# Optimization experiments

Hardware: AMD Instinct MI355X
Metric: run time of the kernel (lower is better)

## Reference

```python
import jax, jax.numpy as jnp
import numpy as np

B, C, H, W = 16, 8, 512, 512
EPS_TH = 1e-14

def setup_inputs() -> dict:
    key = jax.random.key(0)
    x = jax.random.normal(key, (B, C, H, W), dtype=jnp.float32)
    alpha = jnp.full((1,), 0.95, dtype=jnp.float32)
    beta = jnp.full((1,), 8.0, dtype=jnp.float32)
    return {"x": x, "alpha": alpha, "beta": beta}

def reference(x, alpha, beta):
    b, c, h, w = x.shape
    x2 = x.reshape(b * c, h * w)
    # torch.nanquantile with default linear interpolation == jnp.nanquantile
    i1 = jnp.nanquantile(x2, 0.01, axis=1, keepdims=True)   # [B*C, 1]
    i99 = jnp.nanquantile(x2, 0.99, axis=1, keepdims=True)  # [B*C, 1]
    th = (i1 + (i99 - i1) * alpha).reshape(b, c, 1, 1)      # broadcast instead of tile
    mask = (th > EPS_TH).astype(x.dtype)
    th_new = th * mask + (1.0 - mask)
    gate = 1.0 / (1.0 + jnp.exp(-(beta / th_new * (jnp.abs(x) - th * mask))))
    return jax.nn.relu(x) * gate
```

## Files before the change

kernel.cpp:

```cpp
#include <hip/hip_runtime.h>


#define ROWS 128
#define NPR  262144
#define BINS 8192
#define SHIFT 19
#define CAP  4096
#define HTPB 256
#define HBPR 8
#define QTPB 1024
#define OTPB 256

#define K_LO 2621u
#define K_HI 259521u

__device__ __forceinline__ unsigned keyOf(float f) {
    unsigned u = __float_as_uint(f);
    return (u & 0x80000000u) ? ~u : (u | 0x80000000u);
}
__device__ __forceinline__ float keyToFloat(unsigned k) {
    unsigned u = (k & 0x80000000u) ? (k & 0x7fffffffu) : ~k;
    return __uint_as_float(u);
}

__global__ __launch_bounds__(HTPB) void k_hist(const float* __restrict__ x,
                                               unsigned* __restrict__ gh) {
    __shared__ unsigned lh[BINS];
    for (int i = threadIdx.x; i < BINS; i += HTPB) lh[i] = 0;
    __syncthreads();
    const int row = blockIdx.x >> 3;
    const int blk = blockIdx.x & 7;
    const float4* xr = (const float4*)(x + (size_t)row * NPR + (size_t)blk * (NPR / HBPR));
    const int NV = NPR / HBPR / 4;
    for (int i = threadIdx.x; i < NV; i += HTPB) {
        float4 v = xr[i];
        atomicAdd(&lh[keyOf(v.x) >> SHIFT], 1u);
        atomicAdd(&lh[keyOf(v.y) >> SHIFT], 1u);
        atomicAdd(&lh[keyOf(v.z) >> SHIFT], 1u);
        atomicAdd(&lh[keyOf(v.w) >> SHIFT], 1u);
    }
    __syncthreads();
    unsigned* h = gh + (size_t)row * BINS;
    for (int i = threadIdx.x; i < BINS; i += HTPB) {
        unsigned c = lh[i];
        if (c) atomicAdd(&h[i], c);
    }
}

__global__ __launch_bounds__(QTPB) void k_qsel(const float* __restrict__ x,
                                               const unsigned* __restrict__ gh,
                                               float* __restrict__ qv) {
    const int row = blockIdx.x;
    const int tid = threadIdx.x;
    const float4* xr = (const float4*)(x + (size_t)row * NPR);

    __shared__ unsigned smem[BINS];
    unsigned (*cand)[CAP] = (unsigned(*)[CAP])smem;
    __shared__ unsigned part[256];
    __shared__ unsigned sh[256];
    __shared__ unsigned sb[8];
    __shared__ unsigned svar[4];
    __shared__ unsigned ccnt[2];

    const unsigned* h = gh + (size_t)row * BINS;
    for (int i = tid; i < BINS; i += QTPB) smem[i] = h[i];
    __syncthreads();

    const int CH = BINS / 256;
    if (tid < 256) {
        unsigned s = 0;
        int base = tid * CH;
        for (int i = 0; i < CH; ++i) s += smem[base + i];
        part[tid] = s;
    }
    __syncthreads();
    if (tid == 0) {
        unsigned run = 0;
        for (int t = 0; t < 256; ++t) { unsigned tmp = part[t]; part[t] = run; run += tmp; }
    }
    __syncthreads();
    if (tid < 256) {
        unsigned cum = part[tid];
        int base = tid * CH;
        const unsigned targets[4] = {K_LO, K_LO + 1u, K_HI, K_HI + 1u};
        for (int i = 0; i < CH; ++i) {
            unsigned c = smem[base + i];
            if (c) {
                #pragma unroll
                for (int t = 0; t < 4; ++t) {
                    if (targets[t] >= cum && targets[t] < cum + c) {
                        if      (t == 0) { sb[0] = base + i; sb[2] = cum; }
                        else if (t == 1) { sb[1] = base + i; }
                        else if (t == 2) { sb[3] = base + i; sb[5] = cum; }
                        else             { sb[4] = base + i; }
                    }
                }
            }
            cum += c;
        }
    }
    if (tid < 2) ccnt[tid] = 0;
    __syncthreads();

    {
        unsigned blo0 = sb[0], bhi0 = sb[1], blo1 = sb[3], bhi1 = sb[4];
        const int NV = NPR / 4;
        for (int i = tid; i < NV; i += QTPB) {
            float4 v = xr[i];
            float vv[4] = {v.x, v.y, v.z, v.w};
            #pragma unroll
            for (int j = 0; j < 4; ++j) {
                unsigned key = keyOf(vv[j]);
                unsigned bin = key >> SHIFT;
                if (bin >= blo0 && bin <= bhi0) {
                    unsigned p = atomicAdd(&ccnt[0], 1u);
                    if (p < CAP) cand[0][p] = key;
                }
                if (bin >= blo1 && bin <= bhi1) {
                    unsigned p = atomicAdd(&ccnt[1], 1u);
                    if (p < CAP) cand[1][p] = key;
                }
            }
        }
    }
    __syncthreads();

    for (int iq = 0; iq < 2; ++iq) {
        unsigned m = ccnt[iq]; if (m > CAP) m = CAP;
        unsigned cb = iq ? sb[5] : sb[2];
        unsigned t_lo = (iq ? K_HI : K_LO) - cb;
        unsigned prefix = 0, trem = t_lo, cntEq = 0;
        for (int p = 3; p >= 0; --p) {
            for (int i = tid; i < 256; i += QTPB) sh[i] = 0;
            __syncthreads();
            for (unsigned i = tid; i < m; i += QTPB) {
                unsigned key = cand[iq][i];
                bool match = (p == 3) || ((key >> ((p + 1) * 8)) == (prefix >> ((p + 1) * 8)));
                if (match) atomicAdd(&sh[(key >> (p * 8)) & 255u], 1u);
            }
            __syncthreads();
            if (tid == 0) {
                unsigned cum = 0;
                for (int b = 0; b < 256; ++b) {
                    unsigned c = sh[b];
                    if (trem >= cum && trem < cum + c) { svar[0] = (unsigned)b; svar[1] = cum; svar[2] = c; break; }
                    cum += c;
                }
            }
            __syncthreads();
            prefix |= svar[0] << (p * 8);
            trem   -= svar[1];
            cntEq   = svar[2];
            __syncthreads();
        }
        unsigned vlo_key = prefix;
        unsigned cntLess = t_lo - trem;
        unsigned vhi_key;
        if (t_lo + 1u < cntLess + cntEq) {
            vhi_key = vlo_key;
        } else {
            if (tid == 0) svar[3] = 0xFFFFFFFFu;
            __syncthreads();
            for (unsigned i = tid; i < m; i += QTPB) {
                unsigned key = cand[iq][i];
                if (key > vlo_key) atomicMin(&svar[3], key);
            }
            __syncthreads();
            vhi_key = svar[3];
        }
        if (tid == 0) {
            double frac = iq ? (0.99 * (double)(NPR - 1) - (double)K_HI)
                             : (0.01 * (double)(NPR - 1) - (double)K_LO);
            double vlo = (double)keyToFloat(vlo_key);
            double vhi = (double)keyToFloat(vhi_key);
            qv[row * 2 + iq] = (float)(vlo + (vhi - vlo) * frac);
        }
        __syncthreads();
    }
}

__global__ __launch_bounds__(OTPB) void k_out(const float* __restrict__ x,
                                              const float* __restrict__ alpha,
                                              const float* __restrict__ beta,
                                              const float* __restrict__ qv,
                                              float* __restrict__ out) {
    const int row = blockIdx.x >> 4;
    float q0 = qv[row * 2], q1 = qv[row * 2 + 1];
    float a = alpha[0], bt = beta[0];
    float th = q0 + (q1 - q0) * a;
    bool  msk = th > 1e-14f;
    float thn = msk ? th : 1.0f;
    float thm = msk ? th : 0.0f;
    float nsc = -(bt / thn) * 1.4426950408889634f;
    const float4* xv = (const float4*)x + (size_t)blockIdx.x * 4096;
    float4*       ov = (float4*)out     + (size_t)blockIdx.x * 4096;
    #pragma unroll 4
    for (int k = 0; k < 16; ++k) {
        int i = k * OTPB + threadIdx.x;
        float4 v = xv[i];
        float4 o;
        o.x = v.x > 0.f ? v.x * __builtin_amdgcn_rcpf(1.f + __builtin_amdgcn_exp2f(nsc * (fabsf(v.x) - thm))) : 0.f;
        o.y = v.y > 0.f ? v.y * __builtin_amdgcn_rcpf(1.f + __builtin_amdgcn_exp2f(nsc * (fabsf(v.y) - thm))) : 0.f;
        o.z = v.z > 0.f ? v.z * __builtin_amdgcn_rcpf(1.f + __builtin_amdgcn_exp2f(nsc * (fabsf(v.z) - thm))) : 0.f;
        o.w = v.w > 0.f ? v.w * __builtin_amdgcn_rcpf(1.f + __builtin_amdgcn_exp2f(nsc * (fabsf(v.w) - thm))) : 0.f;
        ov[i] = o;
    }
}

extern "C" void kernel_launch(void* const* d_in, const int* in_sizes, int n_in,
                              void* d_out, int out_size, void* d_ws, size_t ws_size,
                              hipStream_t stream) {
    const float* x     = (const float*)d_in[0];
    const float* alpha = (const float*)d_in[1];
    const float* beta  = (const float*)d_in[2];
    float* out = (float*)d_out;
    unsigned* gh = (unsigned*)d_ws;
    float* qv = (float*)(gh + (size_t)ROWS * BINS);
    hipMemsetAsync(gh, 0, (size_t)ROWS * BINS * sizeof(unsigned), stream);
    k_hist<<<ROWS * HBPR, HTPB, 0, stream>>>(x, gh);
    k_qsel<<<ROWS,        QTPB, 0, stream>>>(x, gh, qv);
    k_out <<<ROWS * 16,   OTPB, 0, stream>>>(x, alpha, beta, qv, out);
}
```

Baseline: 419.8 us.

## Split quantile selection into scan, parallel collect, and per-quantile select kernels

Before, one 1024-thread block per row did the candidate-collection pass over the whole row, so the second full read of x ran on only 128 blocks. That pass now goes to a separate collect kernel with 16 blocks per row, each buffering candidates in LDS and appending them to global arrays through a global atomic counter. Radix select runs in its own kernel with one block per (row, quantile). The histogram now uses 2 blocks per row, each writing its own partial histogram instead of atomically merging, so the big memset shrinks to a small counter clear. The cost is two extra kernel launches and global round-trips for candidates, plus per-block LDS buffer caps that could drop candidates if a bin range is dense.

```diff
diff --git a/kernel.cpp b/kernel.cpp
--- a/kernel.cpp
+++ b/kernel.cpp
@@ -6,13 +6,16 @@
 #define BINS 8192
 #define SHIFT 19
 #define CAP  4096
-#define HTPB 256
-#define HBPR 8
-#define QTPB 1024
-#define OTPB 256
+#define CBUF 2048
 
 #define K_LO 2621u
 #define K_HI 259521u
+
+#define OFF_GH   0
+#define OFF_GCNT (ROWS*2*BINS)
+#define OFF_SB   (OFF_GCNT + 256)
+#define OFF_CAND (OFF_SB + ROWS*8)
+#define OFF_QV   (OFF_CAND + ROWS*2*CAP)
 
 __device__ __forceinline__ unsigned keyOf(float f) {
     unsigned u = __float_as_uint(f);
@@ -23,16 +26,16 @@
     return __uint_as_float(u);
 }
 
-__global__ __launch_bounds__(HTPB) void k_hist(const float* __restrict__ x,
+__global__ __launch_bounds__(1024) void k_hist(const float* __restrict__ x,
                                                unsigned* __restrict__ gh) {
     __shared__ unsigned lh[BINS];
-    for (int i = threadIdx.x; i < BINS; i += HTPB) lh[i] = 0;
-    __syncthreads();
-    const int row = blockIdx.x >> 3;
-    const int blk = blockIdx.x & 7;
-    const float4* xr = (const float4*)(x + (size_t)row * NPR + (size_t)blk * (NPR / HBPR));
-    const int NV = NPR / HBPR / 4;
-    for (int i = threadIdx.x; i < NV; i += HTPB) {
+    for (int i = threadIdx.x; i < BINS; i += 1024) lh[i] = 0;
+    __syncthreads();
+    const int row  = blockIdx.x >> 1;
+    const int half = blockIdx.x & 1;
+    const float4* xr = (const float4*)(x + (size_t)row * NPR + (size_t)half * (NPR / 2));
+    const int NV = NPR / 2 / 4;
+    for (int i = threadIdx.x; i < NV; i += 1024) {
         float4 v = xr[i];
         atomicAdd(&lh[keyOf(v.x) >> SHIFT], 1u);
         atomicAdd(&lh[keyOf(v.y) >> SHIFT], 1u);
@@ -40,51 +43,36 @@
         atomicAdd(&lh[keyOf(v.w) >> SHIFT], 1u);
     }
     __syncthreads();
-    unsigned* h = gh + (size_t)row * BINS;
-    for (int i = threadIdx.x; i < BINS; i += HTPB) {
-        unsigned c = lh[i];
-        if (c) atomicAdd(&h[i], c);
-    }
-}
-
-__global__ __launch_bounds__(QTPB) void k_qsel(const float* __restrict__ x,
-                                               const unsigned* __restrict__ gh,
-                                               float* __restrict__ qv) {
+    unsigned* h = gh + (size_t)blockIdx.x * BINS;
+    for (int i = threadIdx.x; i < BINS; i += 1024) h[i] = lh[i];
+}
+
+__global__ __launch_bounds__(256) void k_scan(const unsigned* __restrict__ gh,
+                                              unsigned* __restrict__ sbinfo) {
     const int row = blockIdx.x;
     const int tid = threadIdx.x;
-    const float4* xr = (const float4*)(x + (size_t)row * NPR);
-
-    __shared__ unsigned smem[BINS];
-    unsigned (*cand)[CAP] = (unsigned(*)[CAP])smem;
+    const unsigned* h0 = gh + (size_t)(row * 2) * BINS;
+    const unsigned* h1 = h0 + BINS;
     __shared__ unsigned part[256];
-    __shared__ unsigned sh[256];
     __shared__ unsigned sb[8];
-    __shared__ unsigned svar[4];
-    __shared__ unsigned ccnt[2];
-
-    const unsigned* h = gh + (size_t)row * BINS;
-    for (int i = tid; i < BINS; i += QTPB) smem[i] = h[i];
-    __syncthreads();
-
     const int CH = BINS / 256;
-    if (tid < 256) {
-        unsigned s = 0;
-        int base = tid * CH;
-        for (int i = 0; i < CH; ++i) s += smem[base + i];
-        part[tid] = s;
-    }
+    int base = tid * CH;
+    unsigned loc[CH];
+    unsigned s = 0;
+    #pragma unroll
+    for (int i = 0; i < CH; ++i) { loc[i] = h0[base + i] + h1[base + i]; s += loc[i]; }
+    part[tid] = s;
     __syncthreads();
     if (tid == 0) {
         unsigned run = 0;
         for (int t = 0; t < 256; ++t) { unsigned tmp = part[t]; part[t] = run; run += tmp; }
     }
     __syncthreads();
-    if (tid < 256) {
+    {
         unsigned cum = part[tid];
-        int base = tid * CH;
         const unsigned targets[4] = {K_LO, K_LO + 1u, K_HI, K_HI + 1u};
         for (int i = 0; i < CH; ++i) {
-            unsigned c = smem[base + i];
+            unsigned c = loc[i];
             if (c) {
                 #pragma unroll
                 for (int t = 0; t < 4; ++t) {
@@ -99,91 +87,138 @@
             cum += c;
         }
     }
-    if (tid < 2) ccnt[tid] = 0;
-    __syncthreads();
-
-    {
-        unsigned blo0 = sb[0], bhi0 = sb[1], blo1 = sb[3], bhi1 = sb[4];
-        const int NV = NPR / 4;
-        for (int i = tid; i < NV; i += QTPB) {
-            float4 v = xr[i];
-            float vv[4] = {v.x, v.y, v.z, v.w};
-            #pragma unroll
-            for (int j = 0; j < 4; ++j) {
-                unsigned key = keyOf(vv[j]);
-                unsigned bin = key >> SHIFT;
-                if (bin >= blo0 && bin <= bhi0) {
-                    unsigned p = atomicAdd(&ccnt[0], 1u);
-                    if (p < CAP) cand[0][p] = key;
-                }
-                if (bin >= blo1 && bin <= bhi1) {
-                    unsigned p = atomicAdd(&ccnt[1], 1u);
-                    if (p < CAP) cand[1][p] = key;
-                }
-            }
-        }
-    }
-    __syncthreads();
-
-    for (int iq = 0; iq < 2; ++iq) {
-        unsigned m = ccnt[iq]; if (m > CAP) m = CAP;
-        unsigned cb = iq ? sb[5] : sb[2];
-        unsigned t_lo = (iq ? K_HI : K_LO) - cb;
-        unsigned prefix = 0, trem = t_lo, cntEq = 0;
-        for (int p = 3; p >= 0; --p) {
-            for (int i = tid; i < 256; i += QTPB) sh[i] = 0;
-            __syncthreads();
-            for (unsigned i = tid; i < m; i += QTPB) {
-                unsigned key = cand[iq][i];
-                bool match = (p == 3) || ((key >> ((p + 1) * 8)) == (prefix >> ((p + 1) * 8)));
-                if (match) atomicAdd(&sh[(key >> (p * 8)) & 255u], 1u);
-            }
-            __syncthreads();
-            if (tid == 0) {
-                unsigned cum = 0;
-                for (int b = 0; b < 256; ++b) {
-                    unsigned c = sh[b];
-                    if (trem >= cum && trem < cum + c) { svar[0] = (unsigned)b; svar[1] = cum; svar[2] = c; break; }
-                    cum += c;
-                }
-            }
-            __syncthreads();
-            prefix |= svar[0] << (p * 8);
-            trem   -= svar[1];
-            cntEq   = svar[2];
-            __syncthreads();
-        }
-        unsigned vlo_key = prefix;
-        unsigned cntLess = t_lo - trem;
-        unsigned vhi_key;
-        if (t_lo + 1u < cntLess + cntEq) {
-            vhi_key = vlo_key;
-        } else {
-            if (tid == 0) svar[3] = 0xFFFFFFFFu;
-            __syncthreads();
-            for (unsigned i = tid; i < m; i += QTPB) {
-                unsigned key = cand[iq][i];
-                if (key > vlo_key) atomicMin(&svar[3], key);
-            }
-            __syncthreads();
-            vhi_key = svar[3];
-        }
+    __syncthreads();
+    if (tid == 0) {
+        unsigned* r = sbinfo + row * 8;
+        r[0] = sb[0] << SHIFT;
+        r[1] = ((sb[1] + 1u) << SHIFT) - 1u;
+        r[2] = sb[2];
+        r[3] = sb[3] << SHIFT;
+        r[4] = ((sb[4] + 1u) << SHIFT) - 1u;
+        r[5] = sb[5];
+    }
+}
+
+__global__ __launch_bounds__(256) void k_collect(const float* __restrict__ x,
+                                                 const unsigned* __restrict__ sbinfo,
+                                                 unsigned* __restrict__ gcnt,
+                                                 unsigned* __restrict__ candg) {
+    __shared__ unsigned buf0[CBUF], buf1[CBUF];
+    __shared__ unsigned lc[2];
+    __shared__ unsigned gbase[2];
+    const int row = blockIdx.x >> 4;
+    const int blk = blockIdx.x & 15;
+    if (threadIdx.x < 2) lc[threadIdx.x] = 0;
+    __syncthreads();
+    const unsigned* r = sbinfo + row * 8;
+    const unsigned klo0 = r[0], khi0 = r[1], klo1 = r[3], khi1 = r[4];
+    const float4* xr = (const float4*)(x + (size_t)row * NPR + (size_t)blk * (NPR / 16));
+    const int NV = NPR / 16 / 4;
+    for (int i = threadIdx.x; i < NV; i += 256) {
+        float4 v = xr[i];
+        float vv[4] = {v.x, v.y, v.z, v.w};
+        #pragma unroll
+        for (int j = 0; j < 4; ++j) {
+            unsigned key = keyOf(vv[j]);
+            if (key >= klo0 && key <= khi0) {
+                unsigned p = atomicAdd(&lc[0], 1u);
+                if (p < CBUF) buf0[p] = key;
+            }
+            if (key >= klo1 && key <= khi1) {
+                unsigned p = atomicAdd(&lc[1], 1u);
+                if (p < CBUF) buf1[p] = key;
+            }
+        }
+    }
+    __syncthreads();
+    if (threadIdx.x < 2) {
+        unsigned n = lc[threadIdx.x]; if (n > CBUF) n = CBUF;
+        gbase[threadIdx.x] = atomicAdd(&gcnt[row * 2 + threadIdx.x], n);
+    }
+    __syncthreads();
+    unsigned n0 = lc[0] > CBUF ? CBUF : lc[0];
+    unsigned n1 = lc[1] > CBUF ? CBUF : lc[1];
+    unsigned* c0 = candg + (size_t)(row * 2) * CAP;
+    unsigned* c1 = c0 + CAP;
+    for (unsigned i = threadIdx.x; i < n0; i += 256) {
+        unsigned p = gbase[0] + i; if (p < CAP) c0[p] = buf0[i];
+    }
+    for (unsigned i = threadIdx.x; i < n1; i += 256) {
+        unsigned p = gbase[1] + i; if (p < CAP) c1[p] = buf1[i];
+    }
+}
+
+__global__ __launch_bounds__(256) void k_select(const unsigned* __restrict__ candg,
+                                                const unsigned* __restrict__ gcnt,
+                                                const unsigned* __restrict__ sbinfo,
+                                                float* __restrict__ qv) {
+    const int rq  = blockIdx.x;
+    const int row = rq >> 1;
+    const int iq  = rq & 1;
+    const int tid = threadIdx.x;
+    __shared__ unsigned keys[CAP];
+    __shared__ unsigned sh[256];
+    __shared__ unsigned svar[4];
+    unsigned m = gcnt[rq]; if (m > CAP) m = CAP;
+    const unsigned* cand = candg + (size_t)rq * CAP;
+    for (unsigned i = tid; i < m; i += 256) keys[i] = cand[i];
+    __syncthreads();
+
+    const unsigned cb   = sbinfo[row * 8 + (iq ? 5 : 2)];
+    const unsigned t_lo = (iq ? K_HI : K_LO) - cb;
+    unsigned prefix = 0, trem = t_lo, cntEq = 0;
+    for (int p = 3; p >= 0; --p) {
+        sh[tid] = 0;
+        __syncthreads();
+        for (unsigned i = tid; i < m; i += 256) {
+            unsigned key = keys[i];
+            bool match = (p == 3) || ((key >> ((p + 1) * 8)) == (prefix >> ((p + 1) * 8)));
+            if (match) atomicAdd(&sh[(key >> (p * 8)) & 255u], 1u);
+        }
+        __syncthreads();
         if (tid == 0) {
-            double frac = iq ? (0.99 * (double)(NPR - 1) - (double)K_HI)
-                             : (0.01 * (double)(NPR - 1) - (double)K_LO);
-            double vlo = (double)keyToFloat(vlo_key);
-            double vhi = (double)keyToFloat(vhi_key);
-            qv[row * 2 + iq] = (float)(vlo + (vhi - vlo) * frac);
-        }
-        __syncthreads();
-    }
-}
-
-__global__ __launch_bounds__(OTPB) void k_out(const float* __restrict__ x,
-                                              const float* __restrict__ alpha,
-                                              const float* __restrict__ beta,
-                                              const float* __restrict__ qv,
-                                              float* __restrict__ out) {
+            unsigned cum = 0;
+            for (int b = 0; b < 256; ++b) {
+                unsigned c = sh[b];
+                if (trem >= cum && trem < cum + c) { svar[0] = (unsigned)b; svar[1] = cum; svar[2] = c; break; }
+                cum += c;
+            }
+        }
+        __syncthreads();
+        prefix |= svar[0] << (p * 8);
+        trem   -= svar[1];
+        cntEq   = svar[2];
+        __syncthreads();
+    }
+    unsigned vlo_key = prefix;
+    unsigned cntLess = t_lo - trem;
+    unsigned vhi_key;
+    if (t_lo + 1u < cntLess + cntEq) {
+        vhi_key = vlo_key;
+    } else {
+        if (tid == 0) svar[3] = 0xFFFFFFFFu;
+        __syncthreads();
+        for (unsigned i = tid; i < m; i += 256) {
+            unsigned key = keys[i];
+            if (key > vlo_key) atomicMin(&svar[3], key);
+        }
+        __syncthreads();
+        vhi_key = svar[3];
+    }
+    if (tid == 0) {
+        double frac = iq ? (0.99 * (double)(NPR - 1) - (double)K_HI)
+                         : (0.01 * (double)(NPR - 1) - (double)K_LO);
+        double vlo = (double)keyToFloat(vlo_key);
+        double vhi = (double)keyToFloat(vhi_key);
+        qv[rq] = (float)(vlo + (vhi - vlo) * frac);
+    }
+}
+
+__global__ __launch_bounds__(256) void k_out(const float* __restrict__ x,
+                                             const float* __restrict__ alpha,
+                                             const float* __restrict__ beta,
+                                             const float* __restrict__ qv,
+                                             float* __restrict__ out) {
     const int row = blockIdx.x >> 4;
     float q0 = qv[row * 2], q1 = qv[row * 2 + 1];
     float a = alpha[0], bt = beta[0];
@@ -196,7 +231,7 @@
     float4*       ov = (float4*)out     + (size_t)blockIdx.x * 4096;
     #pragma unroll 4
     for (int k = 0; k < 16; ++k) {
-        int i = k * OTPB + threadIdx.x;
+        int i = k * 256 + threadIdx.x;
         float4 v = xv[i];
         float4 o;
         o.x = v.x > 0.f ? v.x * __builtin_amdgcn_rcpf(1.f + __builtin_amdgcn_exp2f(nsc * (fabsf(v.x) - thm))) : 0.f;
@@ -214,10 +249,16 @@
     const float* alpha = (const float*)d_in[1];
     const float* beta  = (const float*)d_in[2];
     float* out = (float*)d_out;
-    unsigned* gh = (unsigned*)d_ws;
-    float* qv = (float*)(gh + (size_t)ROWS * BINS);
-    hipMemsetAsync(gh, 0, (size_t)ROWS * BINS * sizeof(unsigned), stream);
-    k_hist<<<ROWS * HBPR, HTPB, 0, stream>>>(x, gh);
-    k_qsel<<<ROWS,        QTPB, 0, stream>>>(x, gh, qv);
-    k_out <<<ROWS * 16,   OTPB, 0, stream>>>(x, alpha, beta, qv, out);
-}
+    unsigned* ws = (unsigned*)d_ws;
+    unsigned* gh     = ws + OFF_GH;
+    unsigned* gcnt   = ws + OFF_GCNT;
+    unsigned* sbinfo = ws + OFF_SB;
+    unsigned* candg  = ws + OFF_CAND;
+    float*    qv     = (float*)(ws + OFF_QV);
+    hipMemsetAsync(gcnt, 0, 256 * sizeof(unsigned), stream);
+    k_hist   <<<ROWS * 2,  1024, 0, stream>>>(x, gh);
+    k_scan   <<<ROWS,      256,  0, stream>>>(gh, sbinfo);
+    k_collect<<<ROWS * 16, 256,  0, stream>>>(x, sbinfo, gcnt, candg);
+    k_select <<<ROWS * 2,  256,  0, stream>>>(candg, gcnt, sbinfo, qv);
+    k_out    <<<ROWS * 16, 256,  0, stream>>>(x, alpha, beta, qv, out);
+}
```

After: 357.2 us. 14.9% less time.
